# Kernel tuning notes

Measured on AMD Instinct MI355X. Metric: run time of the kernel, lower is better.

The kernel has to match this reference:

```python
import jax, jax.numpy as jnp
import numpy as np

N = 50000          # nodes
E = 800000         # edges (before self-loops)
IN_CH = 16
HID = 32
HEADS = 4
NEG_SLOPE = 0.2    # PyG GATConv default leaky_relu slope


def add_self_loops(edge_index, n):
    loops = jnp.arange(n, dtype=edge_index.dtype)
    return jnp.concatenate([edge_index, jnp.stack([loops, loops])], axis=1)


def gat_layer(x, edge_index, W, a_src, a_dst, bias, heads, out_ch, concat):
    """PyG-style GATConv: gather -> attention logits -> segment softmax over dst -> scatter."""
    n = x.shape[0]
    h = (x @ W).reshape(n, heads, out_ch)            # [N, H, C]
    src, dst = edge_index[0], edge_index[1]          # messages flow src -> dst
    alpha_src = (h * a_src).sum(-1)                  # [N, H]
    alpha_dst = (h * a_dst).sum(-1)                  # [N, H]
    e = jax.nn.leaky_relu(alpha_src[src] + alpha_dst[dst], NEG_SLOPE)  # [Etot, H]
    # numerically stable segment softmax over incoming edges of each dst node
    e_max = jax.ops.segment_max(e, dst, num_segments=n)
    e_exp = jnp.exp(e - e_max[dst])
    denom = jax.ops.segment_sum(e_exp, dst, num_segments=n)
    alpha = e_exp / (denom[dst] + 1e-16)             # [Etot, H]
    out = jax.ops.segment_sum(h[src] * alpha[..., None], dst, num_segments=n)  # [N, H, C]
    out = out.reshape(n, heads * out_ch) if concat else out.mean(axis=1)
    return out + bias


def setup_inputs() -> dict:
    key = jax.random.key(0)
    ks = jax.random.split(key, 10)
    x = jax.random.normal(ks[0], (N, IN_CH), dtype=jnp.float32)
    edge_index = jax.random.randint(ks[1], (2, E), 0, N, dtype=jnp.int64)
    s = 0.1
    W1 = jax.random.normal(ks[2], (IN_CH, HEADS * HID), dtype=jnp.float32) * s
    a_src1 = jax.random.normal(ks[3], (1, HEADS, HID), dtype=jnp.float32) * s
    a_dst1 = jax.random.normal(ks[4], (1, HEADS, HID), dtype=jnp.float32) * s
    b1 = jnp.zeros((HEADS * HID,), dtype=jnp.float32)
    W2 = jax.random.normal(ks[5], (HEADS * HID, 2), dtype=jnp.float32) * s
    a_src2 = jax.random.normal(ks[6], (1, 1, 2), dtype=jnp.float32) * s
    a_dst2 = jax.random.normal(ks[7], (1, 1, 2), dtype=jnp.float32) * s
    b2 = jnp.zeros((2,), dtype=jnp.float32)
    return {"x": x, "edge_index": edge_index,
            "W1": W1, "a_src1": a_src1, "a_dst1": a_dst1, "b1": b1,
            "W2": W2, "a_src2": a_src2, "a_dst2": a_dst2, "b2": b2}


def reference(x, edge_index, W1, a_src1, a_dst1, b1, W2, a_src2, a_dst2, b2):
    ei = add_self_loops(edge_index, x.shape[0])
    h = gat_layer(x, ei, W1, a_src1, a_dst1, b1, HEADS, HID, concat=True)
    h = jax.nn.relu(h)
    out = gat_layer(h, ei, W2, a_src2, a_dst2, b2, 1, 2, concat=False)
    return out
```

## Files before the change

### kernel.cpp

```cpp
#include <hip/hip_runtime.h>
#include <hip/hip_bf16.h>

#define N_NODES 50000
#define N_EDGES 800000
#define ETOT    (N_EDGES + N_NODES)
#define STRIDE  64
#define IN_CH   16
#define HID     32
#define HEADS   4
#define C1      (HEADS * HID)
#define NEG     0.2f

#define DEG_BLOCKS ((ETOT / 4 + 255) / 256)
#define NGROUPS    (N_NODES / 4)
#define H1_BLOCKS  2048

typedef unsigned short u16;
typedef unsigned int   u32;

__device__ __forceinline__ float bf2f(u16 b) {
    return __uint_as_float(((u32)b) << 16);
}

__device__ __forceinline__ u16 f2bf(float f) {
    __hip_bfloat16 hb = __float2bfloat16(f);
    return *(u16*)&hb;
}

__device__ __forceinline__ int clampn(int v) {
    return v < 0 ? 0 : (v >= N_NODES ? N_NODES - 1 : v);
}

__device__ __forceinline__ int eidx(const int* ei, int e, int i64, int which) {
    int v = i64 ? ei[2 * (which * N_EDGES + e)] : ei[which * N_EDGES + e];
    return clampn(v);
}

__device__ __forceinline__ float cvt(const void* src, int i, int bf) {
    return bf ? bf2f(((const u16*)src)[i]) : ((const float*)src)[i];
}

__device__ __forceinline__ int probe_bf_wave(const u16* xb) {
    int l = threadIdx.x & 63;
    int my = 0;
#pragma unroll
    for (int k = 0; k < 4; k++) {
        float f = bf2f(xb[l * 4 + k]);
        float a = fabsf(f);
        if (f == 0.0f || (a > 9.5e-7f && a < 1.05e6f)) my++;
    }
#pragma unroll
    for (int m = 32; m; m >>= 1) my += __shfl_xor(my, m);
    return my >= 224;
}

__device__ __forceinline__ int probe_i64_wave(const int* ei32) {
    int l = threadIdx.x & 63;
    int nz = (l < 32 && ei32[2 * l + 1] != 0) ? 1 : 0;
#pragma unroll
    for (int m = 32; m; m >>= 1) nz += __shfl_xor(nz, m);
    return nz == 0;
}

__device__ __forceinline__ void dev_deg(const int* __restrict__ ei,
                                        int* __restrict__ degs,
                                        u32* __restrict__ srp, int blk) {
    int i64 = probe_i64_wave(ei);
    int e0 = (blk * 256 + (int)threadIdx.x) * 4;
    if (e0 >= ETOT) return;
    int s[4], d[4];
#pragma unroll
    for (int j = 0; j < 4; j++) {
        int e = e0 + j;
        if (e < N_EDGES) { s[j] = eidx(ei, e, i64, 0); d[j] = eidx(ei, e, i64, 1); }
        else             { s[j] = d[j] = e - N_EDGES; }
    }
    u32 r[4];
#pragma unroll
    for (int j = 0; j < 4; j++) {
        u32 rr = (u32)atomicAdd(&degs[d[j]], 1) + 1u;
        r[j] = ((u32)s[j] << 16) | (rr > 0xFFFFu ? 0xFFFFu : rr);
    }
    *(uint4*)(srp + e0) = make_uint4(r[0], r[1], r[2], r[3]);
}

__device__ __forceinline__ void dev_fill(const int* __restrict__ ei,
                                         const u32* __restrict__ srp,
                                         u16* __restrict__ csr, int blk) {
    int i64 = probe_i64_wave(ei);
    int e0 = (blk * 256 + (int)threadIdx.x) * 4;
    if (e0 >= ETOT) return;
    uint4 q = *(const uint4*)(srp + e0);
    u32 sr[4] = {q.x, q.y, q.z, q.w};
#pragma unroll
    for (int j = 0; j < 4; j++) {
        int e = e0 + j;
        int d = (e < N_EDGES) ? eidx(ei, e, i64, 1) : (e - N_EDGES);
        u32 r = sr[j] & 0xFFFFu;
        if (r < STRIDE) csr[d * STRIDE + r] = (u16)(sr[j] >> 16);
    }
}

__device__ __forceinline__ void dev_h1(const void* __restrict__ x,
                                       const void* __restrict__ W1,
                                       const void* __restrict__ a_s,
                                       const void* __restrict__ a_d,
                                       u32* __restrict__ h1u,
                                       float* __restrict__ as1,
                                       float* __restrict__ ad1,
                                       float* Ws, float* As, float* Ad, int blk) {
    int bf = probe_bf_wave((const u16*)x);
    if (blk == 0 && threadIdx.x < 4) as1[N_NODES * 4 + threadIdx.x] = -1e30f;
    if (bf) {
        const u32* w32 = (const u32*)W1;
        for (int i = threadIdx.x; i < IN_CH * C1 / 2; i += 256) {
            u32 v = w32[i];
            Ws[2 * i]     = bf2f((u16)(v & 0xFFFF));
            Ws[2 * i + 1] = bf2f((u16)(v >> 16));
        }
        const u32* s32 = (const u32*)a_s;
        const u32* d32 = (const u32*)a_d;
        for (int i = threadIdx.x; i < C1 / 2; i += 256) {
            u32 vs = s32[i], vd = d32[i];
            As[2 * i]     = bf2f((u16)(vs & 0xFFFF));
            As[2 * i + 1] = bf2f((u16)(vs >> 16));
            Ad[2 * i]     = bf2f((u16)(vd & 0xFFFF));
            Ad[2 * i + 1] = bf2f((u16)(vd >> 16));
        }
    } else {
        for (int i = threadIdx.x; i < IN_CH * C1; i += 256) Ws[i] = ((const float*)W1)[i];
        for (int i = threadIdx.x; i < C1; i += 256) {
            As[i] = ((const float*)a_s)[i];
            Ad[i] = ((const float*)a_d)[i];
        }
    }
    __syncthreads();

    int w = threadIdx.x >> 6, l = threadIdx.x & 63;
    int c0 = 2 * l, c1 = 2 * l + 1;
    for (int g = blk; g < NGROUPS; g += H1_BLOCKS) {
        int n = g * 4 + w;
        float xval = (l < IN_CH) ? cvt(x, n * IN_CH + l, bf) : 0.f;
        float acc0 = 0.f, acc1 = 0.f;
#pragma unroll
        for (int k = 0; k < IN_CH; k++) {
            float xk = __shfl(xval, k);
            acc0 += xk * Ws[k * C1 + c0];
            acc1 += xk * Ws[k * C1 + c1];
        }
        h1u[n * 64 + l] = (u32)f2bf(acc0) | ((u32)f2bf(acc1) << 16);

        float ps = acc0 * As[c0] + acc1 * As[c1];
        float pd = acc0 * Ad[c0] + acc1 * Ad[c1];
#pragma unroll
        for (int m = 8; m; m >>= 1) { ps += __shfl_xor(ps, m); pd += __shfl_xor(pd, m); }
        if ((l & 15) == 0) {
            int hd = l >> 4;
            as1[n * 4 + hd] = ps;
            ad1[n * 4 + hd] = pd;
        }
    }
}

__launch_bounds__(256)
__global__ void k_deg(const int* __restrict__ ei, int* __restrict__ degs,
                      u32* __restrict__ srp) {
    dev_deg(ei, degs, srp, blockIdx.x);
}

__launch_bounds__(256)
__global__ void k_fill_h1(const void* __restrict__ x, const int* __restrict__ ei,
                          const void* __restrict__ W1, const void* __restrict__ a_s,
                          const void* __restrict__ a_d, const u32* __restrict__ srp,
                          u16* __restrict__ csr, u32* __restrict__ h1u,
                          float* __restrict__ as1, float* __restrict__ ad1) {
    __shared__ float Ws[IN_CH * C1];
    __shared__ float As[C1], Ad[C1];
    if (blockIdx.x < DEG_BLOCKS) { dev_fill(ei, srp, csr, blockIdx.x); return; }
    dev_h1(x, W1, a_s, a_d, h1u, as1, ad1, Ws, As, Ad, blockIdx.x - DEG_BLOCKS);
}

__launch_bounds__(256)
__global__ void k_fill(const int* __restrict__ ei, const u32* __restrict__ srp,
                       u16* __restrict__ csr) {
    dev_fill(ei, srp, csr, blockIdx.x);
}

__launch_bounds__(256)
__global__ void k_h1_only(const void* __restrict__ x, const void* __restrict__ W1,
                          const void* __restrict__ a_s, const void* __restrict__ a_d,
                          u32* __restrict__ h1u, float* __restrict__ as1,
                          float* __restrict__ ad1) {
    __shared__ float Ws[IN_CH * C1];
    __shared__ float As[C1], Ad[C1];
    dev_h1(x, W1, a_s, a_d, h1u, as1, ad1, Ws, As, Ad, blockIdx.x);
}

__launch_bounds__(256)
__global__ void k_gather1(const void* __restrict__ x,
                          const int* __restrict__ degs, const u16* __restrict__ csr,
                          const u32* __restrict__ h1u,
                          const float* __restrict__ as1, const float* __restrict__ ad1,
                          const void* __restrict__ b1, const void* __restrict__ W2,
                          const void* __restrict__ a2s, const void* __restrict__ a2d,
                          float* __restrict__ h2, float* __restrict__ as2,
                          float* __restrict__ ad2) {
    int bf = probe_bf_wave((const u16*)x);
    int n = blockIdx.x * 4 + (threadIdx.x >> 6);
    int l = threadIdx.x & 63;
    int hd = l >> 4;
    int je = l & 7;
    int jh = (l >> 3) & 3;
    float advb = ad1[n * 4 + jh];
    int deg = degs[n] + 1;
    deg = deg > STRIDE ? STRIDE : deg;
    int nb = (deg + 7) >> 3;
    const u16* row = csr + (size_t)n * STRIDE;
    float acc0 = 0.f, acc1 = 0.f, sw = 0.f;

    for (int b = 0; b < nb; b++) {
        int se = (int)row[b * 8 + je];
        if (se >= N_NODES) se = N_NODES;
        float t = as1[se * 4 + jh] + advb;
        t = t > 0.f ? t : NEG * t;
        float wm = __expf(t);
#pragma unroll
        for (int j = 0; j < 8; j++) {
            int   sj = __shfl(se, j);
            float wj = __shfl(wm, hd * 8 + j);
            u32 p = h1u[sj * 64 + l];
            sw   += wj;
            acc0 += wj * bf2f((u16)(p & 0xFFFF));
            acc1 += wj * bf2f((u16)(p >> 16));
        }
    }

    float inv = 1.0f / sw;
    float v0 = acc0 * inv + cvt(b1, 2 * l, bf);
    float v1 = acc1 * inv + cvt(b1, 2 * l + 1, bf);
    v0 = v0 > 0.f ? v0 : 0.f;
    v1 = v1 > 0.f ? v1 : 0.f;
    float p0 = v0 * cvt(W2, 4 * l,     bf) + v1 * cvt(W2, 4 * l + 2, bf);
    float p1 = v0 * cvt(W2, 4 * l + 1, bf) + v1 * cvt(W2, 4 * l + 3, bf);
#pragma unroll
    for (int d = 32; d; d >>= 1) { p0 += __shfl_down(p0, d); p1 += __shfl_down(p1, d); }
    if (l == 0) {
        h2[n * 2] = p0; h2[n * 2 + 1] = p1;
        as2[n] = p0 * cvt(a2s, 0, bf) + p1 * cvt(a2s, 1, bf);
        ad2[n] = p0 * cvt(a2d, 0, bf) + p1 * cvt(a2d, 1, bf);
    }
}

__launch_bounds__(256)
__global__ void k_gather2(const void* __restrict__ x,
                          const int* __restrict__ degs, const u16* __restrict__ csr,
                          const float* __restrict__ h2, const float* __restrict__ as2,
                          const float* __restrict__ ad2, const void* __restrict__ b2,
                          void* __restrict__ out) {
    int bf = probe_bf_wave((const u16*)x);
    int n = blockIdx.x * 16 + (threadIdx.x >> 4);
    int g = threadIdx.x & 15;
    float adv = ad2[n], a0 = 0.f, a1 = 0.f, sw = 0.f;
    int deg = degs[n] + 1;
    deg = deg > STRIDE ? STRIDE : deg;
    const u16* row = csr + (size_t)n * STRIDE;
    for (int k = g; k < deg; k += 16) {
        int s = (int)row[k];
        float lg = as2[s] + adv;
        lg = lg > 0.f ? lg : NEG * lg;
        float w = __expf(lg);
        float2 hv = ((const float2*)h2)[s];
        a0 += w * hv.x;
        a1 += w * hv.y;
        sw += w;
    }
#pragma unroll
    for (int m = 8; m; m >>= 1) {
        a0 += __shfl_xor(a0, m); a1 += __shfl_xor(a1, m); sw += __shfl_xor(sw, m);
    }
    if (g == 0) {
        float inv = 1.0f / sw;
        float o0 = a0 * inv + cvt(b2, 0, bf);
        float o1 = a1 * inv + cvt(b2, 1, bf);
        if (bf) {
            ((u32*)out)[n] = (u32)f2bf(o0) | ((u32)f2bf(o1) << 16);
        } else {
            ((float2*)out)[n] = make_float2(o0, o1);
        }
    }
}

extern "C" void kernel_launch(void* const* d_in, const int* in_sizes, int n_in,
                              void* d_out, int out_size, void* d_ws, size_t ws_size,
                              hipStream_t stream) {
    const void* x    = d_in[0];
    const int*  ei   = (const int*)d_in[1];
    const void* W1   = d_in[2];
    const void* a_s1 = d_in[3];
    const void* a_d1 = d_in[4];
    const void* b1   = d_in[5];
    const void* W2   = d_in[6];
    const void* a_s2 = d_in[7];
    const void* a_d2 = d_in[8];
    const void* b2   = d_in[9];

    char* p = (char*)d_ws;
    int*   degs = (int*)p;     p += ((size_t)N_NODES * 4 + 255) & ~255;
    u16*   csr  = (u16*)p;     p += (size_t)N_NODES * STRIDE * 2;
    size_t init_bytes = (size_t)(p - (char*)d_ws);
    u32*   h1u  = (u32*)p;     p += (size_t)(N_NODES + 1) * 64 * 4;
    float* as1  = (float*)p;   p += (size_t)(N_NODES + 1) * HEADS * 4;
    float* ad1  = (float*)p;   p += (size_t)N_NODES * HEADS * 4;
    float* h2   = (float*)p;   p += (size_t)N_NODES * 2 * 4;
    float* as2  = (float*)p;   p += (size_t)N_NODES * 4;
    float* ad2  = (float*)p;   p += (size_t)N_NODES * 4;
    size_t base_used = (size_t)(p - (char*)d_ws);
    size_t srp_bytes = (size_t)ETOT * 4;

    hipMemsetAsync(degs, 0xFF, init_bytes, stream);

    if (ws_size >= base_used + srp_bytes) {
        u32* srp = (u32*)p;
        k_deg<<<DEG_BLOCKS, 256, 0, stream>>>(ei, degs, srp);
        k_fill_h1<<<DEG_BLOCKS + H1_BLOCKS, 256, 0, stream>>>(
            x, ei, W1, a_s1, a_d1, srp, csr, h1u, as1, ad1);
    } else {
        u32* srp = h1u;
        k_deg<<<DEG_BLOCKS, 256, 0, stream>>>(ei, degs, srp);
        k_fill<<<DEG_BLOCKS, 256, 0, stream>>>(ei, srp, csr);
        k_h1_only<<<H1_BLOCKS, 256, 0, stream>>>(x, W1, a_s1, a_d1, h1u, as1, ad1);
    }
    k_gather1<<<N_NODES / 4, 256, 0, stream>>>(
        x, degs, csr, h1u, as1, ad1, b1, W2, a_s2, a_d2, h2, as2, ad2);
    k_gather2<<<N_NODES / 16, 256, 0, stream>>>(
        x, degs, csr, h2, as2, ad2, b2, d_out);
}
```

Before: 204.8 us.

## Co-schedule h1 with degree pass, prefetch CSR indices, reduce weight sum once

The h1 projection now runs in the same launch as the degree-counting blocks instead of alongside the CSR fill, and the fill becomes its own launch afterward. In the layer-1 gather, the next batch of neighbor indices is loaded one iteration ahead, and the softmax denominator is accumulated per lane and reduced with shuffles once after the loop instead of being summed inside the inner loop. This aims to overlap independent work, hide index-load latency, and cut per-edge ALU work, at the cost of a few extra registers and a changed launch grouping.

Result: no change. 204.6 us (-0.1%).

```diff
diff --git a/kernel.cpp b/kernel.cpp
--- a/kernel.cpp
+++ b/kernel.cpp
@@ -163,21 +163,22 @@
 }
 
 __launch_bounds__(256)
+__global__ void k_deg_h1(const void* __restrict__ x, const int* __restrict__ ei,
+                         const void* __restrict__ W1, const void* __restrict__ a_s,
+                         const void* __restrict__ a_d,
+                         int* __restrict__ degs, u32* __restrict__ srp,
+                         u32* __restrict__ h1u, float* __restrict__ as1,
+                         float* __restrict__ ad1) {
+    __shared__ float Ws[IN_CH * C1];
+    __shared__ float As[C1], Ad[C1];
+    if (blockIdx.x < DEG_BLOCKS) { dev_deg(ei, degs, srp, blockIdx.x); return; }
+    dev_h1(x, W1, a_s, a_d, h1u, as1, ad1, Ws, As, Ad, blockIdx.x - DEG_BLOCKS);
+}
+
+__launch_bounds__(256)
 __global__ void k_deg(const int* __restrict__ ei, int* __restrict__ degs,
                       u32* __restrict__ srp) {
     dev_deg(ei, degs, srp, blockIdx.x);
-}
-
-__launch_bounds__(256)
-__global__ void k_fill_h1(const void* __restrict__ x, const int* __restrict__ ei,
-                          const void* __restrict__ W1, const void* __restrict__ a_s,
-                          const void* __restrict__ a_d, const u32* __restrict__ srp,
-                          u16* __restrict__ csr, u32* __restrict__ h1u,
-                          float* __restrict__ as1, float* __restrict__ ad1) {
-    __shared__ float Ws[IN_CH * C1];
-    __shared__ float As[C1], Ad[C1];
-    if (blockIdx.x < DEG_BLOCKS) { dev_fill(ei, srp, csr, blockIdx.x); return; }
-    dev_h1(x, W1, a_s, a_d, h1u, as1, ad1, Ws, As, Ad, blockIdx.x - DEG_BLOCKS);
 }
 
 __launch_bounds__(256)
@@ -216,24 +217,32 @@
     deg = deg > STRIDE ? STRIDE : deg;
     int nb = (deg + 7) >> 3;
     const u16* row = csr + (size_t)n * STRIDE;
-    float acc0 = 0.f, acc1 = 0.f, sw = 0.f;
-
+    float acc0 = 0.f, acc1 = 0.f, swd = 0.f;
+
+    int se = (int)row[je];
+    if (se >= N_NODES) se = N_NODES;
     for (int b = 0; b < nb; b++) {
-        int se = (int)row[b * 8 + je];
-        if (se >= N_NODES) se = N_NODES;
+        int se_next = 0xFFFF;
+        if (b + 1 < nb) se_next = (int)row[(b + 1) * 8 + je];
         float t = as1[se * 4 + jh] + advb;
         t = t > 0.f ? t : NEG * t;
         float wm = __expf(t);
+        swd += wm;
 #pragma unroll
         for (int j = 0; j < 8; j++) {
             int   sj = __shfl(se, j);
             float wj = __shfl(wm, hd * 8 + j);
             u32 p = h1u[sj * 64 + l];
-            sw   += wj;
             acc0 += wj * bf2f((u16)(p & 0xFFFF));
             acc1 += wj * bf2f((u16)(p >> 16));
         }
-    }
+        se = se_next >= N_NODES ? N_NODES : se_next;
+    }
+
+    swd += __shfl_xor(swd, 1);
+    swd += __shfl_xor(swd, 2);
+    swd += __shfl_xor(swd, 4);
+    float sw = __shfl(swd, hd * 8);
 
     float inv = 1.0f / sw;
     float v0 = acc0 * inv + cvt(b1, 2 * l, bf);
@@ -321,9 +330,9 @@
 
     if (ws_size >= base_used + srp_bytes) {
         u32* srp = (u32*)p;
-        k_deg<<<DEG_BLOCKS, 256, 0, stream>>>(ei, degs, srp);
-        k_fill_h1<<<DEG_BLOCKS + H1_BLOCKS, 256, 0, stream>>>(
-            x, ei, W1, a_s1, a_d1, srp, csr, h1u, as1, ad1);
+        k_deg_h1<<<DEG_BLOCKS + H1_BLOCKS, 256, 0, stream>>>(
+            x, ei, W1, a_s1, a_d1, degs, srp, h1u, as1, ad1);
+        k_fill<<<DEG_BLOCKS, 256, 0, stream>>>(ei, srp, csr);
     } else {
         u32* srp = h1u;
         k_deg<<<DEG_BLOCKS, 256, 0, stream>>>(ei, degs, srp);
```

## Fuse all stages into one persistent cooperative kernel with grid syncs

Applied to the files above, without the earlier changes.

Replaces the memset plus four separate kernel launches with a single cooperative persistent kernel. It initializes the degree and CSR buffers in-kernel, computes h1, then builds degrees, fills the CSR, and runs both gather layers, separated by grid-wide barriers. The aim is to remove launch gaps and the memset. In exchange, each stage is limited to a grid capped at 2048 blocks that loops over the work, and every stage boundary pays for a grid sync. The old multi-kernel path is kept as a fallback if the cooperative launch fails.

Result: slower. 746.6 us (+264.6%).

```diff
diff --git a/kernel.cpp b/kernel.cpp
--- a/kernel.cpp
+++ b/kernel.cpp
@@ -1,5 +1,8 @@
 #include <hip/hip_runtime.h>
 #include <hip/hip_bf16.h>
+#include <hip/hip_cooperative_groups.h>
+
+namespace cg = cooperative_groups;
 
 #define N_NODES 50000
 #define N_EDGES 800000
@@ -13,7 +16,11 @@
 
 #define DEG_BLOCKS ((ETOT / 4 + 255) / 256)
 #define NGROUPS    (N_NODES / 4)
+#define G2GROUPS   (N_NODES / 16)
 #define H1_BLOCKS  2048
+#define DEGS_PAD  (((size_t)N_NODES * 4 + 255) & ~(size_t)255)
+#define CSR_BYTES ((size_t)N_NODES * STRIDE * 2)
+#define INIT_U4   ((int)((DEGS_PAD + CSR_BYTES) / 16))
 
 typedef unsigned short u16;
 typedef unsigned int   u32;
@@ -108,7 +115,8 @@
                                        u32* __restrict__ h1u,
                                        float* __restrict__ as1,
                                        float* __restrict__ ad1,
-                                       float* Ws, float* As, float* Ad, int blk) {
+                                       float* Ws, float* As, float* Ad,
+                                       int blk, int stride) {
     int bf = probe_bf_wave((const u16*)x);
     if (blk == 0 && threadIdx.x < 4) as1[N_NODES * 4 + threadIdx.x] = -1e30f;
     if (bf) {
@@ -138,7 +146,7 @@
 
     int w = threadIdx.x >> 6, l = threadIdx.x & 63;
     int c0 = 2 * l, c1 = 2 * l + 1;
-    for (int g = blk; g < NGROUPS; g += H1_BLOCKS) {
+    for (int g = blk; g < NGROUPS; g += stride) {
         int n = g * 4 + w;
         float xval = (l < IN_CH) ? cvt(x, n * IN_CH + l, bf) : 0.f;
         float acc0 = 0.f, acc1 = 0.f;
@@ -162,51 +170,15 @@
     }
 }
 
-__launch_bounds__(256)
-__global__ void k_deg(const int* __restrict__ ei, int* __restrict__ degs,
-                      u32* __restrict__ srp) {
-    dev_deg(ei, degs, srp, blockIdx.x);
-}
-
-__launch_bounds__(256)
-__global__ void k_fill_h1(const void* __restrict__ x, const int* __restrict__ ei,
-                          const void* __restrict__ W1, const void* __restrict__ a_s,
-                          const void* __restrict__ a_d, const u32* __restrict__ srp,
-                          u16* __restrict__ csr, u32* __restrict__ h1u,
-                          float* __restrict__ as1, float* __restrict__ ad1) {
-    __shared__ float Ws[IN_CH * C1];
-    __shared__ float As[C1], Ad[C1];
-    if (blockIdx.x < DEG_BLOCKS) { dev_fill(ei, srp, csr, blockIdx.x); return; }
-    dev_h1(x, W1, a_s, a_d, h1u, as1, ad1, Ws, As, Ad, blockIdx.x - DEG_BLOCKS);
-}
-
-__launch_bounds__(256)
-__global__ void k_fill(const int* __restrict__ ei, const u32* __restrict__ srp,
-                       u16* __restrict__ csr) {
-    dev_fill(ei, srp, csr, blockIdx.x);
-}
-
-__launch_bounds__(256)
-__global__ void k_h1_only(const void* __restrict__ x, const void* __restrict__ W1,
-                          const void* __restrict__ a_s, const void* __restrict__ a_d,
-                          u32* __restrict__ h1u, float* __restrict__ as1,
-                          float* __restrict__ ad1) {
-    __shared__ float Ws[IN_CH * C1];
-    __shared__ float As[C1], Ad[C1];
-    dev_h1(x, W1, a_s, a_d, h1u, as1, ad1, Ws, As, Ad, blockIdx.x);
-}
-
-__launch_bounds__(256)
-__global__ void k_gather1(const void* __restrict__ x,
-                          const int* __restrict__ degs, const u16* __restrict__ csr,
-                          const u32* __restrict__ h1u,
-                          const float* __restrict__ as1, const float* __restrict__ ad1,
-                          const void* __restrict__ b1, const void* __restrict__ W2,
-                          const void* __restrict__ a2s, const void* __restrict__ a2d,
-                          float* __restrict__ h2, float* __restrict__ as2,
-                          float* __restrict__ ad2) {
-    int bf = probe_bf_wave((const u16*)x);
-    int n = blockIdx.x * 4 + (threadIdx.x >> 6);
+__device__ __forceinline__ void dev_g1_group(
+        int g, int bf,
+        const int* __restrict__ degs, const u16* __restrict__ csr,
+        const u32* __restrict__ h1u,
+        const float* __restrict__ as1, const float* __restrict__ ad1,
+        const void* __restrict__ b1, const void* __restrict__ W2,
+        const void* __restrict__ a2s, const void* __restrict__ a2d,
+        float* __restrict__ h2, float* __restrict__ as2, float* __restrict__ ad2) {
+    int n = g * 4 + ((int)threadIdx.x >> 6);
     int l = threadIdx.x & 63;
     int hd = l >> 4;
     int je = l & 7;
@@ -251,20 +223,19 @@
     }
 }
 
-__launch_bounds__(256)
-__global__ void k_gather2(const void* __restrict__ x,
-                          const int* __restrict__ degs, const u16* __restrict__ csr,
-                          const float* __restrict__ h2, const float* __restrict__ as2,
-                          const float* __restrict__ ad2, const void* __restrict__ b2,
-                          void* __restrict__ out) {
-    int bf = probe_bf_wave((const u16*)x);
-    int n = blockIdx.x * 16 + (threadIdx.x >> 4);
-    int g = threadIdx.x & 15;
+__device__ __forceinline__ void dev_g2_group(
+        int g, int bf,
+        const int* __restrict__ degs, const u16* __restrict__ csr,
+        const float* __restrict__ h2, const float* __restrict__ as2,
+        const float* __restrict__ ad2, const void* __restrict__ b2,
+        void* __restrict__ out) {
+    int n = g * 16 + ((int)threadIdx.x >> 4);
+    int gg = threadIdx.x & 15;
     float adv = ad2[n], a0 = 0.f, a1 = 0.f, sw = 0.f;
     int deg = degs[n] + 1;
     deg = deg > STRIDE ? STRIDE : deg;
     const u16* row = csr + (size_t)n * STRIDE;
-    for (int k = g; k < deg; k += 16) {
+    for (int k = gg; k < deg; k += 16) {
         int s = (int)row[k];
         float lg = as2[s] + adv;
         lg = lg > 0.f ? lg : NEG * lg;
@@ -278,7 +249,7 @@
     for (int m = 8; m; m >>= 1) {
         a0 += __shfl_xor(a0, m); a1 += __shfl_xor(a1, m); sw += __shfl_xor(sw, m);
     }
-    if (g == 0) {
+    if (gg == 0) {
         float inv = 1.0f / sw;
         float o0 = a0 * inv + cvt(b2, 0, bf);
         float o1 = a1 * inv + cvt(b2, 1, bf);
@@ -288,6 +259,106 @@
             ((float2*)out)[n] = make_float2(o0, o1);
         }
     }
+}
+
+struct KArgs {
+    const void* x; const int* ei;
+    const void* W1; const void* a_s; const void* a_d;
+    const void* b1; const void* W2; const void* a2s; const void* a2d; const void* b2;
+    int* degs; u16* csr; u32* srp; u32* h1u;
+    float* as1; float* ad1; float* h2; float* as2; float* ad2;
+    void* out;
+};
+
+__launch_bounds__(256, 8)
+__global__ void k_all(KArgs a) {
+    cg::grid_group grid = cg::this_grid();
+    __shared__ float Ws[IN_CH * C1];
+    __shared__ float As[C1], Ad[C1];
+    int bid = blockIdx.x;
+    int gsz = gridDim.x;
+
+    {
+        uint4* ip = (uint4*)a.degs;
+        for (int i = bid * 256 + (int)threadIdx.x; i < INIT_U4; i += gsz * 256)
+            ip[i] = make_uint4(~0u, ~0u, ~0u, ~0u);
+    }
+    dev_h1(a.x, a.W1, a.a_s, a.a_d, a.h1u, a.as1, a.ad1, Ws, As, Ad, bid, gsz);
+    int bf = probe_bf_wave((const u16*)a.x);
+    grid.sync();
+
+    for (int b = bid; b < DEG_BLOCKS; b += gsz) dev_deg(a.ei, a.degs, a.srp, b);
+    grid.sync();
+
+    for (int b = bid; b < DEG_BLOCKS; b += gsz) dev_fill(a.ei, a.srp, a.csr, b);
+    grid.sync();
+
+    for (int g = bid; g < NGROUPS; g += gsz)
+        dev_g1_group(g, bf, a.degs, a.csr, a.h1u, a.as1, a.ad1,
+                     a.b1, a.W2, a.a2s, a.a2d, a.h2, a.as2, a.ad2);
+    grid.sync();
+
+    for (int g = bid; g < G2GROUPS; g += gsz)
+        dev_g2_group(g, bf, a.degs, a.csr, a.h2, a.as2, a.ad2, a.b2, a.out);
+}
+
+__launch_bounds__(256)
+__global__ void k_deg(const int* __restrict__ ei, int* __restrict__ degs,
+                      u32* __restrict__ srp) {
+    dev_deg(ei, degs, srp, blockIdx.x);
+}
+
+__launch_bounds__(256)
+__global__ void k_fill_h1(const void* __restrict__ x, const int* __restrict__ ei,
+                          const void* __restrict__ W1, const void* __restrict__ a_s,
+                          const void* __restrict__ a_d, const u32* __restrict__ srp,
+                          u16* __restrict__ csr, u32* __restrict__ h1u,
+                          float* __restrict__ as1, float* __restrict__ ad1) {
+    __shared__ float Ws[IN_CH * C1];
+    __shared__ float As[C1], Ad[C1];
+    if (blockIdx.x < DEG_BLOCKS) { dev_fill(ei, srp, csr, blockIdx.x); return; }
+    dev_h1(x, W1, a_s, a_d, h1u, as1, ad1, Ws, As, Ad,
+           blockIdx.x - DEG_BLOCKS, H1_BLOCKS);
+}
+
+__launch_bounds__(256)
+__global__ void k_fill(const int* __restrict__ ei, const u32* __restrict__ srp,
+                       u16* __restrict__ csr) {
+    dev_fill(ei, srp, csr, blockIdx.x);
+}
+
+__launch_bounds__(256)
+__global__ void k_h1_only(const void* __restrict__ x, const void* __restrict__ W1,
+                          const void* __restrict__ a_s, const void* __restrict__ a_d,
+                          u32* __restrict__ h1u, float* __restrict__ as1,
+                          float* __restrict__ ad1) {
+    __shared__ float Ws[IN_CH * C1];
+    __shared__ float As[C1], Ad[C1];
+    dev_h1(x, W1, a_s, a_d, h1u, as1, ad1, Ws, As, Ad, blockIdx.x, H1_BLOCKS);
+}
+
+__launch_bounds__(256)
+__global__ void k_gather1(const void* __restrict__ x,
+                          const int* __restrict__ degs, const u16* __restrict__ csr,
+                          const u32* __restrict__ h1u,
+                          const float* __restrict__ as1, const float* __restrict__ ad1,
+                          const void* __restrict__ b1, const void* __restrict__ W2,
+                          const void* __restrict__ a2s, const void* __restrict__ a2d,
+                          float* __restrict__ h2, float* __restrict__ as2,
+                          float* __restrict__ ad2) {
+    int bf = probe_bf_wave((const u16*)x);
+    dev_g1_group(blockIdx.x, bf, degs, csr, h1u, as1, ad1, b1, W2, a2s, a2d,
+                 h2, as2, ad2);
+}
+
+__launch_bounds__(256)
+__global__ void k_gather2(const void* __restrict__ x,
+                          const int* __restrict__ degs, const u16* __restrict__ csr,
+                          const float* __restrict__ h2, const float* __restrict__ as2,
+                          const float* __restrict__ ad2, const void* __restrict__ b2,
+                          void* __restrict__ out) {
+    int bf = probe_bf_wave((const u16*)x);
+    dev_g2_group(blockIdx.x, bf, degs, csr, h2, as2, ad2, b2, out);
 }
 
 extern "C" void kernel_launch(void* const* d_in, const int* in_sizes, int n_in,
@@ -305,8 +376,8 @@
     const void* b2   = d_in[9];
 
     char* p = (char*)d_ws;
-    int*   degs = (int*)p;     p += ((size_t)N_NODES * 4 + 255) & ~255;
-    u16*   csr  = (u16*)p;     p += (size_t)N_NODES * STRIDE * 2;
+    int*   degs = (int*)p;     p += DEGS_PAD;
+    u16*   csr  = (u16*)p;     p += CSR_BYTES;
     size_t init_bytes = (size_t)(p - (char*)d_ws);
     u32*   h1u  = (u32*)p;     p += (size_t)(N_NODES + 1) * 64 * 4;
     float* as1  = (float*)p;   p += (size_t)(N_NODES + 1) * HEADS * 4;
@@ -317,21 +388,44 @@
     size_t base_used = (size_t)(p - (char*)d_ws);
     size_t srp_bytes = (size_t)ETOT * 4;
 
-    hipMemsetAsync(degs, 0xFF, init_bytes, stream);
-
     if (ws_size >= base_used + srp_bytes) {
         u32* srp = (u32*)p;
-        k_deg<<<DEG_BLOCKS, 256, 0, stream>>>(ei, degs, srp);
-        k_fill_h1<<<DEG_BLOCKS + H1_BLOCKS, 256, 0, stream>>>(
-            x, ei, W1, a_s1, a_d1, srp, csr, h1u, as1, ad1);
+        hipError_t lerr = hipErrorUnknown;
+        int maxB = 0;
+        hipError_t qerr = hipOccupancyMaxActiveBlocksPerMultiprocessor(
+            &maxB, (const void*)k_all, 256, 0);
+        if (qerr == hipSuccess && maxB >= 1) {
+            int grid = maxB * 256;
+            if (grid > 2048) grid = 2048;
+            KArgs ka;
+            ka.x = x; ka.ei = ei; ka.W1 = W1; ka.a_s = a_s1; ka.a_d = a_d1;
+            ka.b1 = b1; ka.W2 = W2; ka.a2s = a_s2; ka.a2d = a_d2; ka.b2 = b2;
+            ka.degs = degs; ka.csr = csr; ka.srp = srp; ka.h1u = h1u;
+            ka.as1 = as1; ka.ad1 = ad1; ka.h2 = h2; ka.as2 = as2; ka.ad2 = ad2;
+            ka.out = d_out;
+            void* params[] = {&ka};
+            lerr = hipLaunchCooperativeKernel((const void*)k_all, dim3(grid),
+                                              dim3(256), params, 0, stream);
+        }
+        if (lerr != hipSuccess) {
+            hipMemsetAsync(degs, 0xFF, init_bytes, stream);
+            k_deg<<<DEG_BLOCKS, 256, 0, stream>>>(ei, degs, srp);
+            k_fill_h1<<<DEG_BLOCKS + H1_BLOCKS, 256, 0, stream>>>(
+                x, ei, W1, a_s1, a_d1, srp, csr, h1u, as1, ad1);
+            k_gather1<<<NGROUPS, 256, 0, stream>>>(
+                x, degs, csr, h1u, as1, ad1, b1, W2, a_s2, a_d2, h2, as2, ad2);
+            k_gather2<<<G2GROUPS, 256, 0, stream>>>(
+                x, degs, csr, h2, as2, ad2, b2, d_out);
+        }
     } else {
         u32* srp = h1u;
+        hipMemsetAsync(degs, 0xFF, init_bytes, stream);
         k_deg<<<DEG_BLOCKS, 256, 0, stream>>>(ei, degs, srp);
         k_fill<<<DEG_BLOCKS, 256, 0, stream>>>(ei, srp, csr);
         k_h1_only<<<H1_BLOCKS, 256, 0, stream>>>(x, W1, a_s1, a_d1, h1u, as1, ad1);
-    }
-    k_gather1<<<N_NODES / 4, 256, 0, stream>>>(
-        x, degs, csr, h1u, as1, ad1, b1, W2, a_s2, a_d2, h2, as2, ad2);
-    k_gather2<<<N_NODES / 16, 256, 0, stream>>>(
-        x, degs, csr, h2, as2, ad2, b2, d_out);
-}
+        k_gather1<<<NGROUPS, 256, 0, stream>>>(
+            x, degs, csr, h1u, as1, ad1, b1, W2, a_s2, a_d2, h2, as2, ad2);
+        k_gather2<<<G2GROUPS, 256, 0, stream>>>(
+            x, degs, csr, h2, as2, ad2, b2, d_out);
+    }
+}
```
